# Kernel optimization log

Hardware: AMD Instinct MI355X
Metric: run time of the kernel (lower is better)

## Reference

```python
import jax, jax.numpy as jnp
import numpy as np

N, DIM, H, HD = 2048, 1280, 16, 80

def _rotate_half(x):
    x1, x2 = x[..., :x.shape[-1] // 2], x[..., x.shape[-1] // 2:]
    return jnp.concatenate((-x2, x1), axis=-1)

def setup_inputs() -> dict:
    key = jax.random.key(0)
    ks = jax.random.split(key, 6)
    hidden_states = jax.random.normal(ks[0], (N, DIM), dtype=jnp.float32)
    cu_seqlens = jnp.array([0, N // 2, N], dtype=jnp.int32)  # 2 packed segments
    # rotary embeddings: half-dim inverse frequencies, duplicated to head_dim
    inv_freq = 1.0 / (10000.0 ** (np.arange(0, HD // 2, dtype=np.float32) * 2.0 / HD))
    pos = np.arange(N, dtype=np.float32) % (N // 2)  # positions restart per segment
    freqs = pos[:, None] * inv_freq[None, :]           # [N, HD/2]
    emb = jnp.asarray(np.concatenate([freqs, freqs], axis=-1))  # [N, HD]
    cos, sin = jnp.cos(emb), jnp.sin(emb)
    Wqkv = jax.random.normal(ks[1], (DIM, 3 * DIM), dtype=jnp.float32) * (DIM ** -0.5)
    bqkv = jax.random.normal(ks[2], (3 * DIM,), dtype=jnp.float32) * 0.02
    Wproj = jax.random.normal(ks[3], (DIM, DIM), dtype=jnp.float32) * (DIM ** -0.5)
    bproj = jax.random.normal(ks[4], (DIM,), dtype=jnp.float32) * 0.02
    return {"hidden_states": hidden_states, "cu_seqlens": cu_seqlens,
            "cos": cos, "sin": sin, "Wqkv": Wqkv, "bqkv": bqkv,
            "Wproj": Wproj, "bproj": bproj}

def reference(hidden_states, cu_seqlens, cos, sin, Wqkv, bqkv, Wproj, bproj):
    n = hidden_states.shape[0]
    scale = HD ** -0.5
    qkv = (hidden_states @ Wqkv + bqkv).reshape(n, 3, H, HD)
    q, k, v = qkv[:, 0], qkv[:, 1], qkv[:, 2]           # each [N, H, HD]
    # RoPE (fp32), cos/sin broadcast over heads: [N, 1, HD]
    c, s = cos[:, None, :], sin[:, None, :]
    q = q * c + _rotate_half(q) * s
    k = k * c + _rotate_half(k) * s
    # block-diagonal varlen mask from cu_seqlens (per-segment full attention)
    seg_id = jnp.searchsorted(cu_seqlens, jnp.arange(n), side='right')  # [N]
    mask = seg_id[:, None] == seg_id[None, :]                           # [N, N]
    scores = jnp.einsum('qhd,khd->hqk', q, k) * scale                   # [H, N, N]
    scores = jnp.where(mask[None], scores, -jnp.inf)
    attn = jax.nn.softmax(scores.astype(jnp.float32), axis=-1).astype(q.dtype)
    out = jnp.einsum('hqk,khd->qhd', attn, v).reshape(n, H * HD)        # [N, DIM]
    return out @ Wproj + bproj
```

## Files before the change

kernel.cpp:

```cpp
#include <hip/hip_runtime.h>
#include <hip/hip_bf16.h>

constexpr int N_TOK  = 2048;
constexpr int DIM    = 1280;
constexpr int NHEAD  = 16;
constexpr int HD     = 80;
constexpr int QKV_N  = 3 * DIM;

using bf16 = __hip_bfloat16;
typedef __attribute__((ext_vector_type(4)))  float f32x4;
typedef __attribute__((ext_vector_type(16))) float f32x16;
typedef __attribute__((ext_vector_type(8)))  short short8;

__device__ __forceinline__ float b2f(bf16 x) { return __bfloat162float(x); }
__device__ __forceinline__ bf16  f2b(float x) { return __float2bfloat16(x); }

__device__ __forceinline__ unsigned int pk2(float a, float b) {
  __align__(4) bf16 t[2] = {f2b(a), f2b(b)};
  return *reinterpret_cast<unsigned int*>(t);
}

typedef const __attribute__((address_space(1))) unsigned int* gas_u32;
typedef __attribute__((address_space(3))) unsigned int* las_u32;
__device__ __forceinline__ void gload_lds16(const void* g, void* l) {
  __builtin_amdgcn_global_load_lds((gas_u32)g, (las_u32)l, 16, 0, 0);
}

__device__ __forceinline__ void transpose_body(const float* __restrict__ W,
                                               bf16* __restrict__ WT, int K, int N) {
  __shared__ float tile[32][33];
  const int n0 = blockIdx.x * 32, k0 = blockIdx.y * 32;
  const int tc = threadIdx.x & 31, tr = threadIdx.x >> 5;
#pragma unroll
  for (int r = tr; r < 32; r += 8)
    tile[r][tc] = W[(size_t)(k0 + r) * N + n0 + tc];
  __syncthreads();
#pragma unroll
  for (int r = tr; r < 32; r += 8)
    WT[(size_t)(n0 + r) * K + k0 + tc] = f2b(tile[tc][r]);
}

__global__ __launch_bounds__(256)
void prep_kernel(const float* __restrict__ hs, bf16* __restrict__ hsb,
                 const float* __restrict__ Wqkv, bf16* __restrict__ WqkvT,
                 const float* __restrict__ Wproj, bf16* __restrict__ WprojT) {
  if (blockIdx.z == 0) {
    const int bid = blockIdx.y * gridDim.x + blockIdx.x;
    if (bid >= (N_TOK * DIM) / 2048) return;
    const int i = bid * 2048 + threadIdx.x * 8;
    const float4 a = *reinterpret_cast<const float4*>(hs + i);
    const float4 b = *reinterpret_cast<const float4*>(hs + i + 4);
    __align__(16) bf16 w[8] = {f2b(a.x), f2b(a.y), f2b(a.z), f2b(a.w),
                               f2b(b.x), f2b(b.y), f2b(b.z), f2b(b.w)};
    *reinterpret_cast<short8*>(hsb + i) = *reinterpret_cast<const short8*>(w);
  } else if (blockIdx.z == 1) {
    transpose_body(Wqkv, WqkvT, DIM, QKV_N);
  } else {
    if (blockIdx.x >= DIM / 32) return;
    transpose_body(Wproj, WprojT, DIM, DIM);
  }
}

template <int OBF>
__global__ __launch_bounds__(256)
void mfma_gemm(const bf16* __restrict__ A, const bf16* __restrict__ BT,
               const float* __restrict__ bias, void* __restrict__ C,
               int M, int N, int K) {
  __shared__ bf16 As[128 * 64];
  __shared__ bf16 Bs[128 * 64];
  const int tid = threadIdx.x;
  const int wid = tid >> 6, lane = tid & 63;
  const int lm = lane & 15, kg = lane >> 4;
  const int wm = (wid >> 1) * 64, wn = (wid & 1) * 64;
  const int m0 = blockIdx.y * 128, n0 = blockIdx.x * 128;

  const int srow = lane >> 3;
  const int sblk = (lane & 7) ^ srow;

  f32x4 acc[4][4];
#pragma unroll
  for (int i = 0; i < 4; ++i)
#pragma unroll
    for (int j = 0; j < 4; ++j) acc[i][j] = (f32x4){0.f, 0.f, 0.f, 0.f};

  for (int k0 = 0; k0 < K; k0 += 64) {
#pragma unroll
    for (int i = 0; i < 4; ++i) {
      const int slot = i * 4 + wid;
      const int row = slot * 8 + srow;
      gload_lds16(A + (size_t)(m0 + row) * K + k0 + sblk * 8, &As[slot * 512]);
      gload_lds16(BT + (size_t)(n0 + row) * K + k0 + sblk * 8, &Bs[slot * 512]);
    }
    __syncthreads();

#pragma unroll
    for (int kh = 0; kh < 2; ++kh) {
      short8 af[4], bfr[4];
#pragma unroll
      for (int t = 0; t < 4; ++t) {
        const int ar = wm + t * 16 + lm;
        af[t] = *reinterpret_cast<const short8*>(
            &As[ar * 64 + ((kh * 4 + kg) ^ (ar & 7)) * 8]);
        const int br = wn + t * 16 + lm;
        bfr[t] = *reinterpret_cast<const short8*>(
            &Bs[br * 64 + ((kh * 4 + kg) ^ (br & 7)) * 8]);
      }
#pragma unroll
      for (int mi = 0; mi < 4; ++mi)
#pragma unroll
        for (int ni = 0; ni < 4; ++ni)
          acc[mi][ni] = __builtin_amdgcn_mfma_f32_16x16x32_bf16(
              af[mi], bfr[ni], acc[mi][ni], 0, 0, 0);
    }
    __syncthreads();
  }

#pragma unroll
  for (int mi = 0; mi < 4; ++mi) {
#pragma unroll
    for (int ni = 0; ni < 4; ++ni) {
      const int col = n0 + wn + ni * 16 + lm;
      const float bv = bias[col];
#pragma unroll
      for (int r = 0; r < 4; ++r) {
        const int row = m0 + wm + mi * 16 + kg * 4 + r;
        const float v = acc[mi][ni][r] + bv;
        if constexpr (OBF)
          ((bf16*)C)[(size_t)row * N + col] = f2b(v);
        else
          ((float*)C)[(size_t)row * N + col] = v;
      }
    }
  }
}

__global__ __launch_bounds__(256)
void rope_kernel(bf16* __restrict__ qkv, const float* __restrict__ cosb,
                 const float* __restrict__ sinb) {
  const int idx  = blockIdx.x * 256 + threadIdx.x;
  const int d0   = (idx % 5) * 8;
  const int h    = (idx / 5) % NHEAD;
  const int whch = (idx / (5 * NHEAD)) % 2;
  const int n    = idx / (10 * NHEAD);
  const size_t base = (size_t)n * QKV_N + whch * DIM + h * HD;

  short8 a = *reinterpret_cast<const short8*>(qkv + base + d0);
  short8 b = *reinterpret_cast<const short8*>(qkv + base + 40 + d0);
  const float4 c0 = *reinterpret_cast<const float4*>(cosb + n * HD + d0);
  const float4 c1 = *reinterpret_cast<const float4*>(cosb + n * HD + d0 + 4);
  const float4 c2 = *reinterpret_cast<const float4*>(cosb + n * HD + 40 + d0);
  const float4 c3 = *reinterpret_cast<const float4*>(cosb + n * HD + 44 + d0);
  const float4 s0 = *reinterpret_cast<const float4*>(sinb + n * HD + d0);
  const float4 s1 = *reinterpret_cast<const float4*>(sinb + n * HD + d0 + 4);
  const float4 s2 = *reinterpret_cast<const float4*>(sinb + n * HD + 40 + d0);
  const float4 s3 = *reinterpret_cast<const float4*>(sinb + n * HD + 44 + d0);
  const float* cl = &c0.x;
  float cc1[8] = {c0.x, c0.y, c0.z, c0.w, c1.x, c1.y, c1.z, c1.w};
  float cc2[8] = {c2.x, c2.y, c2.z, c2.w, c3.x, c3.y, c3.z, c3.w};
  float ss1[8] = {s0.x, s0.y, s0.z, s0.w, s1.x, s1.y, s1.z, s1.w};
  float ss2[8] = {s2.x, s2.y, s2.z, s2.w, s3.x, s3.y, s3.z, s3.w};
  (void)cl;

  __align__(16) bf16 o1[8], o2[8];
#pragma unroll
  for (int e = 0; e < 8; ++e) {
    const float x1 = b2f(reinterpret_cast<const bf16*>(&a)[e]);
    const float x2 = b2f(reinterpret_cast<const bf16*>(&b)[e]);
    o1[e] = f2b(x1 * cc1[e] - x2 * ss1[e]);
    o2[e] = f2b(x2 * cc2[e] + x1 * ss2[e]);
  }
  *reinterpret_cast<short8*>(qkv + base + d0)      = *reinterpret_cast<const short8*>(o1);
  *reinterpret_cast<short8*>(qkv + base + 40 + d0) = *reinterpret_cast<const short8*>(o2);
}

constexpr int KC   = 64;
constexpr int KSTR = 104;
constexpr int VSTR = 88;
constexpr int VROWS = 96;

__global__ __launch_bounds__(256)
void attn_mfma_kernel(const bf16* __restrict__ qkv, const int* __restrict__ cu,
                      bf16* __restrict__ out, int nseg) {
  __shared__ bf16 Ks[2][KC * KSTR];
  __shared__ bf16 Vt[2][VROWS * VSTR];

  const int p = blockIdx.x;
  const int lidx = (p & 7) * (gridDim.x >> 3) + (p >> 3);
  const int xt  = lidx & 15;
  const int seg = (lidx >> 4) % nseg;
  const int h   = (lidx >> 4) / nseg;

  const int s0 = cu[seg], s1 = cu[seg + 1];
  if (s0 + xt * 128 >= s1) return;

  const int tid  = threadIdx.x;
  const int wid  = tid >> 6, lane = tid & 63;
  const int l31  = lane & 31;
  const int half = lane >> 5;
  const float scale = 0.11180339887498949f;

  const int qrow = s0 + xt * 128 + wid * 32 + l31;

#pragma unroll
  for (int t = 0; t < 2; ++t) {
    const int s = tid + t * 256;
    if (s < 352) {
      const int b = s / 176, rem = s % 176;
      const int r = 80 + rem / 11, sl = rem % 11;
      *reinterpret_cast<short8*>(&Vt[b][r * VSTR + sl * 8]) =
          (short8){0, 0, 0, 0, 0, 0, 0, 0};
    }
  }

  short8 qa[5];
#pragma unroll
  for (int ck = 0; ck < 5; ++ck) {
    const int dbase = ck * 16 + half * 8;
    qa[ck] = (qrow < s1)
        ? *reinterpret_cast<const short8*>(qkv + (size_t)qrow * QKV_N + h * HD + dbase)
        : (short8){0, 0, 0, 0, 0, 0, 0, 0};
  }

  short8 kreg[3], vreg[4];
  const int vgrp = tid / 10, vsl = tid % 10;
  auto issueK = [&](int c) {
    const int k0 = s0 + c * KC;
#pragma unroll
    for (int t = 0; t < 3; ++t) {
      const int s = tid + t * 256;
      if (s < 640) {
        const int r = min(k0 + s / 10, s1 - 1);
        kreg[t] = *reinterpret_cast<const short8*>(
            qkv + (size_t)r * QKV_N + DIM + h * HD + (s % 10) * 8);
      }
    }
  };
  auto commitK = [&](int buf) {
#pragma unroll
    for (int t = 0; t < 3; ++t) {
      const int s = tid + t * 256;
      if (s < 640)
        *reinterpret_cast<short8*>(&Ks[buf][(s / 10) * KSTR + (s % 10) * 8]) =
            kreg[t];
    }
  };
  auto issueV = [&](int c) {
    if (tid < 160) {
      const int k0 = s0 + c * KC;
#pragma unroll
      for (int e = 0; e < 4; ++e) {
        const int r = min(k0 + vgrp * 4 + e, s1 - 1);
        vreg[e] = *reinterpret_cast<const short8*>(
            qkv + (size_t)r * QKV_N + 2 * DIM + h * HD + vsl * 8);
      }
    }
  };
  auto commitV = [&](int buf) {
    if (tid < 160) {
      const int r0 = vgrp * 4;
      const int swz = (vsl & 7) << 3;
#pragma unroll
      for (int de = 0; de < 8; ++de) {
        __align__(8) bf16 w[4] = {reinterpret_cast<const bf16*>(&vreg[0])[de],
                                  reinterpret_cast<const bf16*>(&vreg[1])[de],
                                  reinterpret_cast<const bf16*>(&vreg[2])[de],
                                  reinterpret_cast<const bf16*>(&vreg[3])[de]};
        *reinterpret_cast<uint2*>(&Vt[buf][(vsl * 8 + de) * VSTR + (r0 ^ swz)]) =
            *reinterpret_cast<const uint2*>(w);
      }
    }
  };

  f32x16 oacc[3];
#pragma unroll
  for (int dt = 0; dt < 3; ++dt)
#pragma unroll
    for (int r = 0; r < 16; ++r) oacc[dt][r] = 0.f;
  float m = -1e30f, l = 0.f;
  const int nch = (s1 - s0 + KC - 1) / KC;

  issueK(0);
  issueV(0);
  commitK(0);
  commitV(0);
  if (nch > 1) {
    issueK(1);
    issueV(1);
  }
  __syncthreads();

  for (int c = 0; c < nch; ++c) {
    const int cur = c & 1;
    const int nk = min(KC, s1 - (s0 + c * KC));

    f32x16 sc[2];
    __builtin_amdgcn_s_setprio(1);
#pragma unroll
    for (int kt = 0; kt < 2; ++kt) {
#pragma unroll
      for (int r = 0; r < 16; ++r) sc[kt][r] = 0.f;
#pragma unroll
      for (int ck = 0; ck < 5; ++ck) {
        short8 ka = *reinterpret_cast<const short8*>(
            &Ks[cur][(kt * 32 + l31) * KSTR + ck * 16 + half * 8]);
        sc[kt] = __builtin_amdgcn_mfma_f32_32x32x16_bf16(ka, qa[ck], sc[kt], 0, 0, 0);
      }
    }
    __builtin_amdgcn_s_setprio(0);

    if (c + 1 < nch) {
      commitK(cur ^ 1);
      commitV(cur ^ 1);
    }
    if (c + 2 < nch) {
      issueK(c + 2);
      issueV(c + 2);
    }

#pragma unroll
    for (int kt = 0; kt < 2; ++kt)
#pragma unroll
      for (int r = 0; r < 16; ++r) sc[kt][r] *= scale;
    if (nk < KC) {
#pragma unroll
      for (int kt = 0; kt < 2; ++kt)
#pragma unroll
        for (int r = 0; r < 16; ++r) {
          const int key = kt * 32 + (r & 3) + 8 * (r >> 2) + 4 * half;
          if (key >= nk) sc[kt][r] = -1e30f;
        }
    }
    float rml = sc[0][0];
#pragma unroll
    for (int kt = 0; kt < 2; ++kt)
#pragma unroll
      for (int r = 0; r < 16; ++r)
        if (kt | r) rml = fmaxf(rml, sc[kt][r]);
    if (!__all(rml - m <= 8.0f)) {
      float rm = fmaxf(rml, __shfl_xor(rml, 32));
      const float mnew = fmaxf(m, rm);
      const float fs = __expf(m - mnew);
      m = mnew;
      l *= fs;
#pragma unroll
      for (int dt = 0; dt < 3; ++dt)
#pragma unroll
        for (int r = 0; r < 16; ++r) oacc[dt][r] *= fs;
    }
#pragma unroll
    for (int kt = 0; kt < 2; ++kt)
#pragma unroll
      for (int r = 0; r < 16; ++r) {
        sc[kt][r] = __expf(sc[kt][r] - m);
        l += sc[kt][r];
      }

    unsigned int pbw[4][4];
#pragma unroll
    for (int kt = 0; kt < 2; ++kt) {
      unsigned int w[8];
#pragma unroll
      for (int i = 0; i < 8; ++i) w[i] = pk2(sc[kt][2 * i], sc[kt][2 * i + 1]);
#pragma unroll
      for (int kc2 = 0; kc2 < 2; ++kc2) {
        auto r02 = __builtin_amdgcn_permlane32_swap(w[4 * kc2 + 0],
                                                    w[4 * kc2 + 2], false, false);
        auto r13 = __builtin_amdgcn_permlane32_swap(w[4 * kc2 + 1],
                                                    w[4 * kc2 + 3], false, false);
        pbw[kt * 2 + kc2][0] = r02[0];
        pbw[kt * 2 + kc2][1] = r13[0];
        pbw[kt * 2 + kc2][2] = r02[1];
        pbw[kt * 2 + kc2][3] = r13[1];
      }
    }

    __builtin_amdgcn_s_setprio(1);
#pragma unroll
    for (int kc = 0; kc < 4; ++kc) {
      short8 pb = *reinterpret_cast<const short8*>(&pbw[kc][0]);
#pragma unroll
      for (int dt = 0; dt < 3; ++dt) {
        const int d = dt * 32 + l31;
        short8 va = *reinterpret_cast<const short8*>(
            &Vt[cur][d * VSTR + ((kc * 16 + half * 8) ^ (((d >> 3) & 7) << 3))]);
        oacc[dt] = __builtin_amdgcn_mfma_f32_32x32x16_bf16(va, pb, oacc[dt], 0, 0, 0);
      }
    }
    __builtin_amdgcn_s_setprio(0);

    __syncthreads();
  }

  l += __shfl_xor(l, 32);
  if (qrow < s1) {
    const float inv = 1.f / l;
    bf16* op = out + (size_t)qrow * DIM + h * HD;
#pragma unroll
    for (int dt = 0; dt < 3; ++dt) {
#pragma unroll
      for (int g = 0; g < 4; ++g) {
        const int d = dt * 32 + g * 8 + half * 4;
        if (d < HD) {
          __align__(8) bf16 w[4] = {f2b(oacc[dt][g * 4 + 0] * inv),
                                    f2b(oacc[dt][g * 4 + 1] * inv),
                                    f2b(oacc[dt][g * 4 + 2] * inv),
                                    f2b(oacc[dt][g * 4 + 3] * inv)};
          *reinterpret_cast<uint2*>(op + d) = *reinterpret_cast<const uint2*>(w);
        }
      }
    }
  }
}

extern "C" void kernel_launch(void* const* d_in, const int* in_sizes, int n_in,
                              void* d_out, int out_size, void* d_ws, size_t ws_size,
                              hipStream_t stream) {
  const float* hs    = (const float*)d_in[0];
  const int*   cu    = (const int*)d_in[1];
  const float* cosb  = (const float*)d_in[2];
  const float* sinb  = (const float*)d_in[3];
  const float* Wqkv  = (const float*)d_in[4];
  const float* bqkv  = (const float*)d_in[5];
  const float* Wproj = (const float*)d_in[6];
  const float* bproj = (const float*)d_in[7];

  bf16* qkv      = (bf16*)d_ws;
  bf16* attn_out = qkv + (size_t)N_TOK * QKV_N;
  bf16* WqkvT    = attn_out + (size_t)N_TOK * DIM;
  bf16* WprojT   = WqkvT + (size_t)QKV_N * DIM;
  bf16* hsb      = WprojT + (size_t)DIM * DIM;

  prep_kernel<<<dim3(QKV_N / 32, DIM / 32, 3), 256, 0, stream>>>(
      hs, hsb, Wqkv, WqkvT, Wproj, WprojT);

  mfma_gemm<1><<<dim3(QKV_N / 128, N_TOK / 128), 256, 0, stream>>>(
      hsb, WqkvT, bqkv, qkv, N_TOK, QKV_N, DIM);

  rope_kernel<<<(N_TOK * 2 * NHEAD * 5) / 256, 256, 0, stream>>>(
      qkv, cosb, sinb);

  int nseg = in_sizes[1] - 1;
  int nblk = (N_TOK / 128) * nseg * NHEAD;
  attn_mfma_kernel<<<nblk, 256, 0, stream>>>(qkv, cu, attn_out, nseg);

  mfma_gemm<0><<<dim3(DIM / 128, N_TOK / 128), 256, 0, stream>>>(
      attn_out, WprojT, bproj, d_out, N_TOK, DIM, DIM);
}
```

Measured before the change: 111.4 us.

## Fuse RoPE into attention kernel, apply to Q and K on the fly

Removes the standalone RoPE kernel launch and its read-modify-write pass over Q and K. Q rotation is now done in registers after the Q fragment load, using permlane32_swap to fetch the partner half-dimension elements. K rotation happens during the K-tile global load, before the LDS commit. This trades one full memory pass plus a launch for redundant K rotation work: every query block recomputes RoPE on each K tile it loads and reloads cos/sin from global memory.

```diff
diff --git a/kernel.cpp b/kernel.cpp
--- a/kernel.cpp
+++ b/kernel.cpp
@@ -11,13 +11,14 @@
 typedef __attribute__((ext_vector_type(4)))  float f32x4;
 typedef __attribute__((ext_vector_type(16))) float f32x16;
 typedef __attribute__((ext_vector_type(8)))  short short8;
+typedef unsigned int uint;
 
 __device__ __forceinline__ float b2f(bf16 x) { return __bfloat162float(x); }
 __device__ __forceinline__ bf16  f2b(float x) { return __float2bfloat16(x); }
 
-__device__ __forceinline__ unsigned int pk2(float a, float b) {
+__device__ __forceinline__ uint pk2(float a, float b) {
   __align__(4) bf16 t[2] = {f2b(a), f2b(b)};
-  return *reinterpret_cast<unsigned int*>(t);
+  return *reinterpret_cast<uint*>(t);
 }
 
 typedef const __attribute__((address_space(1))) unsigned int* gas_u32;
@@ -134,45 +135,6 @@
   }
 }
 
-__global__ __launch_bounds__(256)
-void rope_kernel(bf16* __restrict__ qkv, const float* __restrict__ cosb,
-                 const float* __restrict__ sinb) {
-  const int idx  = blockIdx.x * 256 + threadIdx.x;
-  const int d0   = (idx % 5) * 8;
-  const int h    = (idx / 5) % NHEAD;
-  const int whch = (idx / (5 * NHEAD)) % 2;
-  const int n    = idx / (10 * NHEAD);
-  const size_t base = (size_t)n * QKV_N + whch * DIM + h * HD;
-
-  short8 a = *reinterpret_cast<const short8*>(qkv + base + d0);
-  short8 b = *reinterpret_cast<const short8*>(qkv + base + 40 + d0);
-  const float4 c0 = *reinterpret_cast<const float4*>(cosb + n * HD + d0);
-  const float4 c1 = *reinterpret_cast<const float4*>(cosb + n * HD + d0 + 4);
-  const float4 c2 = *reinterpret_cast<const float4*>(cosb + n * HD + 40 + d0);
-  const float4 c3 = *reinterpret_cast<const float4*>(cosb + n * HD + 44 + d0);
-  const float4 s0 = *reinterpret_cast<const float4*>(sinb + n * HD + d0);
-  const float4 s1 = *reinterpret_cast<const float4*>(sinb + n * HD + d0 + 4);
-  const float4 s2 = *reinterpret_cast<const float4*>(sinb + n * HD + 40 + d0);
-  const float4 s3 = *reinterpret_cast<const float4*>(sinb + n * HD + 44 + d0);
-  const float* cl = &c0.x;
-  float cc1[8] = {c0.x, c0.y, c0.z, c0.w, c1.x, c1.y, c1.z, c1.w};
-  float cc2[8] = {c2.x, c2.y, c2.z, c2.w, c3.x, c3.y, c3.z, c3.w};
-  float ss1[8] = {s0.x, s0.y, s0.z, s0.w, s1.x, s1.y, s1.z, s1.w};
-  float ss2[8] = {s2.x, s2.y, s2.z, s2.w, s3.x, s3.y, s3.z, s3.w};
-  (void)cl;
-
-  __align__(16) bf16 o1[8], o2[8];
-#pragma unroll
-  for (int e = 0; e < 8; ++e) {
-    const float x1 = b2f(reinterpret_cast<const bf16*>(&a)[e]);
-    const float x2 = b2f(reinterpret_cast<const bf16*>(&b)[e]);
-    o1[e] = f2b(x1 * cc1[e] - x2 * ss1[e]);
-    o2[e] = f2b(x2 * cc2[e] + x1 * ss2[e]);
-  }
-  *reinterpret_cast<short8*>(qkv + base + d0)      = *reinterpret_cast<const short8*>(o1);
-  *reinterpret_cast<short8*>(qkv + base + 40 + d0) = *reinterpret_cast<const short8*>(o2);
-}
-
 constexpr int KC   = 64;
 constexpr int KSTR = 104;
 constexpr int VSTR = 88;
@@ -180,6 +142,7 @@
 
 __global__ __launch_bounds__(256)
 void attn_mfma_kernel(const bf16* __restrict__ qkv, const int* __restrict__ cu,
+                      const float* __restrict__ cosb, const float* __restrict__ sinb,
                       bf16* __restrict__ out, int nseg) {
   __shared__ bf16 Ks[2][KC * KSTR];
   __shared__ bf16 Vt[2][VROWS * VSTR];
@@ -212,36 +175,105 @@
     }
   }
 
-  short8 qa[5];
-#pragma unroll
-  for (int ck = 0; ck < 5; ++ck) {
-    const int dbase = ck * 16 + half * 8;
-    qa[ck] = (qrow < s1)
+  short8 qraw[5];
+  const int nclamp = min(qrow, s1 - 1);
+#pragma unroll
+  for (int j = 0; j < 5; ++j) {
+    const int dbase = j * 16 + half * 8;
+    qraw[j] = (qrow < s1)
         ? *reinterpret_cast<const short8*>(qkv + (size_t)qrow * QKV_N + h * HD + dbase)
         : (short8){0, 0, 0, 0, 0, 0, 0, 0};
   }
-
-  short8 kreg[3], vreg[4];
+  short8 part[5];
+#pragma unroll
+  for (int w = 0; w < 4; ++w) {
+    const uint d0 = reinterpret_cast<const uint*>(&qraw[0])[w];
+    const uint d1 = reinterpret_cast<const uint*>(&qraw[1])[w];
+    const uint d2 = reinterpret_cast<const uint*>(&qraw[2])[w];
+    const uint d3 = reinterpret_cast<const uint*>(&qraw[3])[w];
+    const uint d4 = reinterpret_cast<const uint*>(&qraw[4])[w];
+    auto s1p = __builtin_amdgcn_permlane32_swap(d2, d0, false, false);
+    auto s2p = __builtin_amdgcn_permlane32_swap(d4, d2, false, false);
+    auto s3p = __builtin_amdgcn_permlane32_swap(d0, d3, false, false);
+    auto s4p = __builtin_amdgcn_permlane32_swap(d3, d1, false, false);
+    auto s5p = __builtin_amdgcn_permlane32_swap(d1, d4, false, false);
+    reinterpret_cast<uint*>(&part[0])[w] = half ? s3p[0] : s1p[1];
+    reinterpret_cast<uint*>(&part[1])[w] = half ? s5p[0] : s4p[1];
+    reinterpret_cast<uint*>(&part[2])[w] = half ? s1p[0] : s2p[1];
+    reinterpret_cast<uint*>(&part[3])[w] = half ? s4p[0] : s3p[1];
+    reinterpret_cast<uint*>(&part[4])[w] = half ? s2p[0] : s5p[1];
+  }
+  short8 qa[5];
+  {
+    const float* cq = cosb + nclamp * HD;
+    const float* sq = sinb + nclamp * HD;
+#pragma unroll
+    for (int j = 0; j < 5; ++j) {
+      const int dbase = j * 16 + half * 8;
+      float cv[8], sv[8];
+      *reinterpret_cast<float4*>(&cv[0]) = *reinterpret_cast<const float4*>(cq + dbase);
+      *reinterpret_cast<float4*>(&cv[4]) = *reinterpret_cast<const float4*>(cq + dbase + 4);
+      *reinterpret_cast<float4*>(&sv[0]) = *reinterpret_cast<const float4*>(sq + dbase);
+      *reinterpret_cast<float4*>(&sv[4]) = *reinterpret_cast<const float4*>(sq + dbase + 4);
+      const float sgn = (dbase < 40) ? -1.f : 1.f;
+      __align__(16) bf16 o[8];
+#pragma unroll
+      for (int e = 0; e < 8; ++e) {
+        const float x  = b2f(reinterpret_cast<const bf16*>(&qraw[j])[e]);
+        const float xp = b2f(reinterpret_cast<const bf16*>(&part[j])[e]);
+        o[e] = f2b(x * cv[e] + sgn * xp * sv[e]);
+      }
+      qa[j] = *reinterpret_cast<const short8*>(o);
+    }
+  }
+
+  short8 kq1[2], kq2[2];
+  short8 vreg[4];
   const int vgrp = tid / 10, vsl = tid % 10;
   auto issueK = [&](int c) {
     const int k0 = s0 + c * KC;
 #pragma unroll
-    for (int t = 0; t < 3; ++t) {
+    for (int t = 0; t < 2; ++t) {
       const int s = tid + t * 256;
-      if (s < 640) {
-        const int r = min(k0 + s / 10, s1 - 1);
-        kreg[t] = *reinterpret_cast<const short8*>(
-            qkv + (size_t)r * QKV_N + DIM + h * HD + (s % 10) * 8);
+      if (s < 320) {
+        const int r = s / 5, sl0 = s % 5;
+        const int rr = min(k0 + r, s1 - 1);
+        const bf16* kp = qkv + (size_t)rr * QKV_N + DIM + h * HD;
+        const short8 x1 = *reinterpret_cast<const short8*>(kp + sl0 * 8);
+        const short8 x2 = *reinterpret_cast<const short8*>(kp + 40 + sl0 * 8);
+        const float* cp = cosb + rr * HD;
+        const float* sp = sinb + rr * HD;
+        float c1[8], c2[8], z1[8], z2[8];
+        *reinterpret_cast<float4*>(&c1[0]) = *reinterpret_cast<const float4*>(cp + sl0 * 8);
+        *reinterpret_cast<float4*>(&c1[4]) = *reinterpret_cast<const float4*>(cp + sl0 * 8 + 4);
+        *reinterpret_cast<float4*>(&c2[0]) = *reinterpret_cast<const float4*>(cp + 40 + sl0 * 8);
+        *reinterpret_cast<float4*>(&c2[4]) = *reinterpret_cast<const float4*>(cp + 44 + sl0 * 8);
+        *reinterpret_cast<float4*>(&z1[0]) = *reinterpret_cast<const float4*>(sp + sl0 * 8);
+        *reinterpret_cast<float4*>(&z1[4]) = *reinterpret_cast<const float4*>(sp + sl0 * 8 + 4);
+        *reinterpret_cast<float4*>(&z2[0]) = *reinterpret_cast<const float4*>(sp + 40 + sl0 * 8);
+        *reinterpret_cast<float4*>(&z2[4]) = *reinterpret_cast<const float4*>(sp + 44 + sl0 * 8);
+        __align__(16) bf16 y1[8], y2[8];
+#pragma unroll
+        for (int e = 0; e < 8; ++e) {
+          const float f1 = b2f(reinterpret_cast<const bf16*>(&x1)[e]);
+          const float f2v = b2f(reinterpret_cast<const bf16*>(&x2)[e]);
+          y1[e] = f2b(f1 * c1[e] - f2v * z1[e]);
+          y2[e] = f2b(f2v * c2[e] + f1 * z2[e]);
+        }
+        kq1[t] = *reinterpret_cast<const short8*>(y1);
+        kq2[t] = *reinterpret_cast<const short8*>(y2);
       }
     }
   };
   auto commitK = [&](int buf) {
 #pragma unroll
-    for (int t = 0; t < 3; ++t) {
+    for (int t = 0; t < 2; ++t) {
       const int s = tid + t * 256;
-      if (s < 640)
-        *reinterpret_cast<short8*>(&Ks[buf][(s / 10) * KSTR + (s % 10) * 8]) =
-            kreg[t];
+      if (s < 320) {
+        const int r = s / 5, sl0 = s % 5;
+        *reinterpret_cast<short8*>(&Ks[buf][r * KSTR + sl0 * 8]) = kq1[t];
+        *reinterpret_cast<short8*>(&Ks[buf][r * KSTR + 40 + sl0 * 8]) = kq2[t];
+      }
     }
   };
   auto issueV = [&](int c) {
@@ -355,10 +387,10 @@
         l += sc[kt][r];
       }
 
-    unsigned int pbw[4][4];
+    uint pbw[4][4];
 #pragma unroll
     for (int kt = 0; kt < 2; ++kt) {
-      unsigned int w[8];
+      uint w[8];
 #pragma unroll
       for (int i = 0; i < 8; ++i) w[i] = pk2(sc[kt][2 * i], sc[kt][2 * i + 1]);
 #pragma unroll
@@ -436,12 +468,9 @@
   mfma_gemm<1><<<dim3(QKV_N / 128, N_TOK / 128), 256, 0, stream>>>(
       hsb, WqkvT, bqkv, qkv, N_TOK, QKV_N, DIM);
 
-  rope_kernel<<<(N_TOK * 2 * NHEAD * 5) / 256, 256, 0, stream>>>(
-      qkv, cosb, sinb);
-
   int nseg = in_sizes[1] - 1;
   int nblk = (N_TOK / 128) * nseg * NHEAD;
-  attn_mfma_kernel<<<nblk, 256, 0, stream>>>(qkv, cu, attn_out, nseg);
+  attn_mfma_kernel<<<nblk, 256, 0, stream>>>(qkv, cu, cosb, sinb, attn_out, nseg);
 
   mfma_gemm<0><<<dim3(DIM / 128, N_TOK / 128), 256, 0, stream>>>(
       attn_out, WprojT, bproj, d_out, N_TOK, DIM, DIM);
```

After: 123.1 us. +10.5%, slower.
